# Optimization experiments

Measured on AMD Instinct MI355X. Metric: run time of the kernel, lower is better.

The kernel has to match this reference:

```python
import jax, jax.numpy as jnp
import numpy as np

MARGIN = 0.3
BIG = 9999999.0


def setup_inputs() -> dict:
    key = jax.random.key(0)
    k1, k2 = jax.random.split(key)
    emb = jax.random.normal(k1, (4096, 2048), dtype=jnp.float32)
    label = jax.random.randint(k2, (4096,), 0, 64, dtype=jnp.int64 if jax.config.jax_enable_x64 else jnp.int32)
    return {"emb": emb, "label": label}


def euclidean_dist(x, y):
    xx = jnp.sum(x * x, axis=1, keepdims=True)          # [m,1]
    yy = jnp.sum(y * y, axis=1, keepdims=True).T        # [1,n]
    dist = xx + yy - 2.0 * (x @ y.T)                    # [m,n]
    return jnp.sqrt(jnp.clip(dist, 1e-12, None))


def reference(emb, label):
    mat_dist = euclidean_dist(emb, emb)                 # [N,N]
    mat_sim = (label[:, None] == label[None, :]).astype(mat_dist.dtype)
    # batch-hard mining: top-1 of masked sorts == masked max / min reductions
    dist_ap = jnp.max(mat_dist - BIG * (1.0 - mat_sim), axis=1)  # hardest positive
    dist_an = jnp.min(mat_dist + BIG * mat_sim, axis=1)          # hardest negative
    # MarginRankingLoss(dist_an, dist_ap, y=1): mean(relu(margin - (dist_an - dist_ap)))
    loss = jnp.mean(jax.nn.relu(MARGIN - (dist_an - dist_ap)))
    prec = jnp.mean((dist_an > dist_ap).astype(jnp.float32))
    return (loss, prec)
```

## Files before the change

### kernel.cpp

```cpp
#include <hip/hip_runtime.h>

#define N_ROWS 4096
#define D_K    2048
#define BM 256
#define BK 32
#define NT (D_K / BK)
#define MARGIN 0.3f

typedef unsigned short u16;
typedef __attribute__((ext_vector_type(8))) short bf16x8;
typedef __attribute__((ext_vector_type(4))) float f32x4;

__device__ __forceinline__ void stage16(const u16* src, u16* dst) {
    __builtin_amdgcn_global_load_lds((const __attribute__((address_space(1))) unsigned int*)src,
                                     (__attribute__((address_space(3))) unsigned int*)dst, 16, 0, 0);
}

__device__ __forceinline__ u16 f2bf(float f) {
    unsigned u = __float_as_uint(f);
    u += 0x7fffu + ((u >> 16) & 1u);
    return (u16)(u >> 16);
}

__global__ __launch_bounds__(256) void prep_kernel(
    const float* __restrict__ emb, u16* __restrict__ embB,
    float* __restrict__ xx, unsigned* __restrict__ ap2, unsigned* __restrict__ an2)
{
    const int row = blockIdx.x;
    const int t = threadIdx.x;
    const float4* src = (const float4*)(emb + (size_t)row * D_K);
    ushort4* dst = (ushort4*)(embB + (size_t)row * D_K);
    float s = 0.f;
#pragma unroll
    for (int i = 0; i < 2; ++i) {
        float4 v = src[t + i * 256];
        s = fmaf(v.x, v.x, s);
        s = fmaf(v.y, v.y, s);
        s = fmaf(v.z, v.z, s);
        s = fmaf(v.w, v.w, s);
        ushort4 o;
        o.x = f2bf(v.x); o.y = f2bf(v.y); o.z = f2bf(v.z); o.w = f2bf(v.w);
        dst[t + i * 256] = o;
    }
#pragma unroll
    for (int off = 32; off >= 1; off >>= 1) s += __shfl_down(s, off, 64);
    __shared__ float red[4];
    if ((t & 63) == 0) red[t >> 6] = s;
    __syncthreads();
    if (t == 0) {
        xx[row] = red[0] + red[1] + red[2] + red[3];
        ap2[row] = 0u;
        an2[row] = 0x7f7fffffu;
    }
}

#define LDv(p) (*(const bf16x8*)(p))
#define BARRIER()  __builtin_amdgcn_s_barrier()
#define VMW_(n)    asm volatile("s_waitcnt vmcnt(" #n ")" ::: "memory")
#define VMW(n)     VMW_(n)

#define STAGE32(B3_, KTE_) do {                       \
    stage16(gA0 + (KTE_), lA + (B3_) * 8192);         \
    stage16(gA1 + (KTE_), lA + (B3_) * 8192 + 4096);  \
    stage16(gB0 + (KTE_), lB + (B3_) * 8192);         \
    stage16(gB1 + (KTE_), lB + (B3_) * 8192 + 4096);  \
} while (0)

#define KT32(B_, T_)                                                                  \
  {                                                                                   \
    const bool ok = ((T_) + 2 < NT);                                                  \
    if (ok) { STAGE32(((B_) + 2) % 3, ((T_) + 2) * BK); }                             \
    bf16x8 aq[8], bq[4];                                                              \
    _Pragma("unroll")                                                                 \
    for (int n = 0; n < 4; ++n)                                                       \
        bq[n] = LDv(BB + (B_) * 16384 + bOff + n * 1024 + kx);                        \
    _Pragma("unroll")                                                                 \
    for (int m = 0; m < 8; ++m)                                                       \
        aq[m] = LDv(AB + (B_) * 16384 + aOff + m * 1024 + kx);                        \
    __builtin_amdgcn_s_setprio(1);                                                    \
    _Pragma("unroll")                                                                 \
    for (int m = 0; m < 8; ++m)                                                       \
        _Pragma("unroll")                                                             \
        for (int n = 0; n < 4; ++n)                                                   \
            acc[m][n] = __builtin_amdgcn_mfma_f32_16x16x32_bf16(aq[m], bq[n], acc[m][n], 0, 0, 0); \
    __builtin_amdgcn_s_setprio(0);                                                    \
    if (ok) { VMW(4); } else { VMW(0); }                                              \
    BARRIER();                                                                        \
  }

__global__ __launch_bounds__(512, 2) void gram_reduce_kernel(
    const u16* __restrict__ embB, const float* __restrict__ xx,
    const int* __restrict__ lab, unsigned* __restrict__ ap2, unsigned* __restrict__ an2)
{
    __shared__ u16 Ash[3 * BM * BK];
    __shared__ u16 Bsh[3 * BM * BK];
    __shared__ int labR[BM], labC[BM];
    __shared__ float xxR[BM], xxC[BM];

    const int tid = threadIdx.x;
    const int bid = blockIdx.x;
    const int swz = (bid & 7) * 32 + (bid >> 3);
    const int bm = swz >> 4, bn = swz & 15;
    const int row0 = bm * BM, col0 = bn * BM;

    const int csw = ((tid & 3) ^ ((tid >> 2) & 3)) * 8;
    const int srow = tid >> 2;
    const u16* gA0 = embB + (size_t)(row0 + srow) * D_K + csw;
    const u16* gA1 = embB + (size_t)(row0 + 128 + srow) * D_K + csw;
    const u16* gB0 = embB + (size_t)(col0 + srow) * D_K + csw;
    const u16* gB1 = embB + (size_t)(col0 + 128 + srow) * D_K + csw;
    u16* lA = Ash + tid * 8;
    u16* lB = Bsh + tid * 8;

    const int l = tid & 63, w = tid >> 6;
    const int wr = w >> 2, wc = w & 3;
    const int fr = l & 15, fkb = l >> 4;
    const int kx = ((fkb ^ (fr & 3)) * 16);
    const char* AB = (const char*)Ash;
    const char* BB = (const char*)Bsh;
    const int aOff = wr * 8192 + fr * 64;
    const int bOff = (wc >> 1) * 8192 + (wc & 1) * 4096 + fr * 64;

    f32x4 acc[8][4];
#pragma unroll
    for (int m = 0; m < 8; ++m)
#pragma unroll
        for (int n = 0; n < 4; ++n) acc[m][n] = (f32x4){0.f, 0.f, 0.f, 0.f};

    STAGE32(0, 0);
    STAGE32(1, BK);
    VMW(4);
    BARRIER();

    for (int ii = 0; ii < 21; ++ii) {
        const int t3 = 3 * ii;
        KT32(0, t3)
        KT32(1, t3 + 1)
        KT32(2, t3 + 2)
    }
    KT32(0, 63)

    if (tid < 256) { labR[tid] = lab[row0 + tid]; xxR[tid] = xx[row0 + tid]; }
    else           { int u2 = tid - 256; labC[u2] = lab[col0 + u2]; xxC[u2] = xx[col0 + u2]; }
    __syncthreads();

    const int rgrp = l >> 4;
#pragma unroll
    for (int m = 0; m < 8; ++m) {
#pragma unroll
        for (int r = 0; r < 4; ++r) {
            const int il = wr * 128 + m * 16 + rgrp * 4 + r;
            const int li = labR[il];
            const float xi = xxR[il];
            float apv = 0.f, anv = __FLT_MAX__;
#pragma unroll
            for (int n = 0; n < 4; ++n) {
                const int jl = wc * 64 + n * 16 + fr;
                float d2 = xi + xxC[jl] - 2.f * acc[m][n][r];
                d2 = fmaxf(d2, 1e-12f);
                const bool same = (labC[jl] == li);
                apv = same ? fmaxf(apv, d2) : apv;
                anv = same ? anv : fminf(anv, d2);
            }
#pragma unroll
            for (int off = 1; off < 16; off <<= 1) {
                apv = fmaxf(apv, __shfl_xor(apv, off, 64));
                anv = fminf(anv, __shfl_xor(anv, off, 64));
            }
            if (fr == 0) {
                atomicMax(&ap2[row0 + il], __float_as_uint(apv));
                atomicMin(&an2[row0 + il], __float_as_uint(anv));
            }
        }
    }
}

__global__ __launch_bounds__(256) void finalize_kernel(
    const unsigned* __restrict__ ap2, const unsigned* __restrict__ an2, float* __restrict__ out)
{
    const int t = threadIdx.x;
    float ls = 0.f, ps = 0.f;
    for (int i = t; i < N_ROWS; i += 256) {
        const float ap = sqrtf(__uint_as_float(ap2[i]));
        const float an = sqrtf(__uint_as_float(an2[i]));
        ls += fmaxf(MARGIN - an + ap, 0.f);
        ps += (an > ap) ? 1.f : 0.f;
    }
#pragma unroll
    for (int off = 32; off >= 1; off >>= 1) {
        ls += __shfl_down(ls, off, 64);
        ps += __shfl_down(ps, off, 64);
    }
    __shared__ float rl[4], rp[4];
    if ((t & 63) == 0) { rl[t >> 6] = ls; rp[t >> 6] = ps; }
    __syncthreads();
    if (t == 0) {
        out[0] = (rl[0] + rl[1] + rl[2] + rl[3]) * (1.f / N_ROWS);
        out[1] = (rp[0] + rp[1] + rp[2] + rp[3]) * (1.f / N_ROWS);
    }
}

extern "C" void kernel_launch(void* const* d_in, const int* in_sizes, int n_in,
                              void* d_out, int out_size, void* d_ws, size_t ws_size,
                              hipStream_t stream)
{
    const float* emb = (const float*)d_in[0];
    const int* lab = (const int*)d_in[1];
    float* out = (float*)d_out;

    char* ws = (char*)d_ws;
    u16* embB   = (u16*)ws;
    float* xx   = (float*)(ws + (size_t)N_ROWS * D_K * 2);
    unsigned* ap2 = (unsigned*)(ws + (size_t)N_ROWS * D_K * 2 + N_ROWS * 4);
    unsigned* an2 = (unsigned*)(ws + (size_t)N_ROWS * D_K * 2 + 2 * (size_t)N_ROWS * 4);

    prep_kernel<<<N_ROWS, 256, 0, stream>>>(emb, embB, xx, ap2, an2);
    dim3 grid((N_ROWS / BM) * (N_ROWS / BM));
    gram_reduce_kernel<<<grid, 512, 0, stream>>>(embB, xx, lab, ap2, an2);
    finalize_kernel<<<1, 256, 0, stream>>>(ap2, an2, out);
}
```

Before: 91.49 us.

## Shrink GEMM block tile to 128x256 with four waves per block

Changes the Gram-matrix block tile from 256x256 with 8 waves to 128x256 with 4 waves, doubling the grid to 512 blocks. All four waves now share the same A rows and each takes a 64-column slice of B. The LDS staging layout, swizzle pattern and wait counts are updated to match. The aim is to halve LDS use per block and give the scheduler more blocks for occupancy and load balance across CUs. The cost is less reuse per block, since more global and L2 traffic is needed for the A and B panels.

```diff
diff --git a/kernel.cpp b/kernel.cpp
--- a/kernel.cpp
+++ b/kernel.cpp
@@ -2,9 +2,10 @@
 
 #define N_ROWS 4096
 #define D_K    2048
-#define BM 256
-#define BK 32
-#define NT (D_K / BK)
+#define BMR 128
+#define BNC 256
+#define BK  32
+#define NT  (D_K / BK)
 #define MARGIN 0.3f
 
 typedef unsigned short u16;
@@ -59,11 +60,13 @@
 #define VMW_(n)    asm volatile("s_waitcnt vmcnt(" #n ")" ::: "memory")
 #define VMW(n)     VMW_(n)
 
-#define STAGE32(B3_, KTE_) do {                       \
-    stage16(gA0 + (KTE_), lA + (B3_) * 8192);         \
-    stage16(gA1 + (KTE_), lA + (B3_) * 8192 + 4096);  \
-    stage16(gB0 + (KTE_), lB + (B3_) * 8192);         \
-    stage16(gB1 + (KTE_), lB + (B3_) * 8192 + 4096);  \
+#define STAGE32(B3_, KTE_) do {                        \
+    stage16(gA0 + (KTE_), lA + (B3_) * 4096);          \
+    stage16(gA1 + (KTE_), lA + (B3_) * 4096 + 2048);   \
+    stage16(gB0 + (KTE_), lB + (B3_) * 8192);          \
+    stage16(gB1 + (KTE_), lB + (B3_) * 8192 + 2048);   \
+    stage16(gB2 + (KTE_), lB + (B3_) * 8192 + 4096);   \
+    stage16(gB3 + (KTE_), lB + (B3_) * 8192 + 6144);   \
 } while (0)
 
 #define KT32(B_, T_)                                                                  \
@@ -76,7 +79,7 @@
         bq[n] = LDv(BB + (B_) * 16384 + bOff + n * 1024 + kx);                        \
     _Pragma("unroll")                                                                 \
     for (int m = 0; m < 8; ++m)                                                       \
-        aq[m] = LDv(AB + (B_) * 16384 + aOff + m * 1024 + kx);                        \
+        aq[m] = LDv(AB + (B_) * 8192 + aOff + m * 1024 + kx);                         \
     __builtin_amdgcn_s_setprio(1);                                                    \
     _Pragma("unroll")                                                                 \
     for (int m = 0; m < 8; ++m)                                                       \
@@ -84,42 +87,43 @@
         for (int n = 0; n < 4; ++n)                                                   \
             acc[m][n] = __builtin_amdgcn_mfma_f32_16x16x32_bf16(aq[m], bq[n], acc[m][n], 0, 0, 0); \
     __builtin_amdgcn_s_setprio(0);                                                    \
-    if (ok) { VMW(4); } else { VMW(0); }                                              \
+    if (ok) { VMW(6); } else { VMW(0); }                                              \
     BARRIER();                                                                        \
   }
 
-__global__ __launch_bounds__(512, 2) void gram_reduce_kernel(
+__global__ __launch_bounds__(256, 2) void gram_reduce_kernel(
     const u16* __restrict__ embB, const float* __restrict__ xx,
     const int* __restrict__ lab, unsigned* __restrict__ ap2, unsigned* __restrict__ an2)
 {
-    __shared__ u16 Ash[3 * BM * BK];
-    __shared__ u16 Bsh[3 * BM * BK];
-    __shared__ int labR[BM], labC[BM];
-    __shared__ float xxR[BM], xxC[BM];
+    __shared__ u16 Ash[3 * BMR * BK];
+    __shared__ u16 Bsh[3 * BNC * BK];
+    __shared__ int labR[BMR], labC[BNC];
+    __shared__ float xxR[BMR], xxC[BNC];
 
     const int tid = threadIdx.x;
     const int bid = blockIdx.x;
-    const int swz = (bid & 7) * 32 + (bid >> 3);
+    const int swz = (bid & 7) * 64 + (bid >> 3);
     const int bm = swz >> 4, bn = swz & 15;
-    const int row0 = bm * BM, col0 = bn * BM;
-
-    const int csw = ((tid & 3) ^ ((tid >> 2) & 3)) * 8;
+    const int row0 = bm * BMR, col0 = bn * BNC;
+
+    const int csw = ((tid & 3) ^ ((tid >> 3) & 3)) * 8;
     const int srow = tid >> 2;
     const u16* gA0 = embB + (size_t)(row0 + srow) * D_K + csw;
-    const u16* gA1 = embB + (size_t)(row0 + 128 + srow) * D_K + csw;
+    const u16* gA1 = embB + (size_t)(row0 + 64 + srow) * D_K + csw;
     const u16* gB0 = embB + (size_t)(col0 + srow) * D_K + csw;
-    const u16* gB1 = embB + (size_t)(col0 + 128 + srow) * D_K + csw;
+    const u16* gB1 = embB + (size_t)(col0 + 64 + srow) * D_K + csw;
+    const u16* gB2 = embB + (size_t)(col0 + 128 + srow) * D_K + csw;
+    const u16* gB3 = embB + (size_t)(col0 + 192 + srow) * D_K + csw;
     u16* lA = Ash + tid * 8;
     u16* lB = Bsh + tid * 8;
 
     const int l = tid & 63, w = tid >> 6;
-    const int wr = w >> 2, wc = w & 3;
     const int fr = l & 15, fkb = l >> 4;
-    const int kx = ((fkb ^ (fr & 3)) * 16);
+    const int kx = (fkb ^ ((fr >> 1) & 3)) * 16;
     const char* AB = (const char*)Ash;
     const char* BB = (const char*)Bsh;
-    const int aOff = wr * 8192 + fr * 64;
-    const int bOff = (wc >> 1) * 8192 + (wc & 1) * 4096 + fr * 64;
+    const int aOff = fr * 64;
+    const int bOff = w * 4096 + fr * 64;
 
     f32x4 acc[8][4];
 #pragma unroll
@@ -129,7 +133,7 @@
 
     STAGE32(0, 0);
     STAGE32(1, BK);
-    VMW(4);
+    VMW(6);
     BARRIER();
 
     for (int ii = 0; ii < 21; ++ii) {
@@ -140,8 +144,8 @@
     }
     KT32(0, 63)
 
-    if (tid < 256) { labR[tid] = lab[row0 + tid]; xxR[tid] = xx[row0 + tid]; }
-    else           { int u2 = tid - 256; labC[u2] = lab[col0 + u2]; xxC[u2] = xx[col0 + u2]; }
+    { int u2 = tid; labC[u2] = lab[col0 + u2]; xxC[u2] = xx[col0 + u2]; }
+    if (tid < 128) { labR[tid] = lab[row0 + tid]; xxR[tid] = xx[row0 + tid]; }
     __syncthreads();
 
     const int rgrp = l >> 4;
@@ -149,13 +153,13 @@
     for (int m = 0; m < 8; ++m) {
 #pragma unroll
         for (int r = 0; r < 4; ++r) {
-            const int il = wr * 128 + m * 16 + rgrp * 4 + r;
+            const int il = m * 16 + rgrp * 4 + r;
             const int li = labR[il];
             const float xi = xxR[il];
             float apv = 0.f, anv = __FLT_MAX__;
 #pragma unroll
             for (int n = 0; n < 4; ++n) {
-                const int jl = wc * 64 + n * 16 + fr;
+                const int jl = w * 64 + n * 16 + fr;
                 float d2 = xi + xxC[jl] - 2.f * acc[m][n][r];
                 d2 = fmaxf(d2, 1e-12f);
                 const bool same = (labC[jl] == li);
@@ -215,7 +219,7 @@
     unsigned* an2 = (unsigned*)(ws + (size_t)N_ROWS * D_K * 2 + 2 * (size_t)N_ROWS * 4);
 
     prep_kernel<<<N_ROWS, 256, 0, stream>>>(emb, embB, xx, ap2, an2);
-    dim3 grid((N_ROWS / BM) * (N_ROWS / BM));
-    gram_reduce_kernel<<<grid, 512, 0, stream>>>(embB, xx, lab, ap2, an2);
+    dim3 grid((N_ROWS / BMR) * (N_ROWS / BNC));
+    gram_reduce_kernel<<<grid, 256, 0, stream>>>(embB, xx, lab, ap2, an2);
     finalize_kernel<<<1, 256, 0, stream>>>(ap2, an2, out);
 }
```

After: 100.2 us. 1.1x slower.
